# Kernel optimization log

Hardware: AMD Instinct MI355X
Metric: run time of the kernel (lower is better)

The kernel has to match this reference:

```python
import jax, jax.numpy as jnp
import numpy as np
from jax import lax


def _ln(x, gamma, beta, eps=1e-5):
    m = jnp.mean(x, -1, keepdims=True)
    v = jnp.mean(jnp.square(x - m), -1, keepdims=True)
    return (x - m) * lax.rsqrt(v + eps) * gamma + beta


def setup_inputs() -> dict:
    key = jax.random.key(0)
    ks = jax.random.split(key, 12)
    B, C, L = 16, 22, 3000
    D, D2, E, T, K = 64, 256, 8, 4, 13
    s = 0.02
    f32 = jnp.float32
    return dict(
        x_stream=jax.random.normal(ks[0], (B, C, L), f32),
        task_ids=jax.random.randint(ks[1], (B,), 0, T),
        conv_w=jax.random.normal(ks[2], (D, C, K), f32) * s,
        conv_b=jnp.zeros((D,), f32),
        cls_token=jax.random.normal(ks[3], (1, 1, D), f32) * s,
        tok_g=jnp.ones((D,), f32), tok_b=jnp.zeros((D,), f32),
        ds_conv_w=jax.random.normal(ks[4], (D2, 1, 1, K), f32) * s,
        ds_conv_b=jnp.zeros((D2,), f32),
        ds_comp_w=jax.random.normal(ks[5], (D2, D2, D), f32) * s,
        ds_comp_b=jnp.zeros((D2,), f32),
        ds_g=jnp.ones((D2,), f32), ds_b=jnp.zeros((D2,), f32),
        task_embed=jax.random.normal(ks[6], (T, D2), f32) * s,
        gate_w=jax.random.normal(ks[7], (2 * D2, E), f32) * s,
        gate_b=jnp.zeros((E,), f32),
        exp_w=jax.random.normal(ks[8], (E, D2, D2), f32) * s,
        exp_b=jnp.zeros((E, D2), f32),
        uni_w=jax.random.normal(ks[9], (D2, D2), f32) * s,
        uni_b=jnp.zeros((D2,), f32),
        out_g=jnp.ones((D2,), f32), out_b=jnp.zeros((D2,), f32),
    )


def reference(x_stream, task_ids, conv_w, conv_b, cls_token, tok_g, tok_b,
              ds_conv_w, ds_conv_b, ds_comp_w, ds_comp_b, ds_g, ds_b,
              task_embed, gate_w, gate_b, exp_w, exp_b, uni_w, uni_b,
              out_g, out_b):
    gelu = lambda x: jax.nn.gelu(x, approximate=False)
    # --- Tokenize1D: conv1d(stride 2, pad 6) -> GELU -> maxpool(3,3) -> cls cat -> LN
    h = lax.conv_general_dilated(x_stream, conv_w, (2,), [(6, 6)],
                                 dimension_numbers=('NCH', 'OIH', 'NCH')) + conv_b[:, None]
    h = gelu(h)
    h = lax.reduce_window(h, -jnp.inf, lax.max, (1, 1, 3), (1, 1, 3), 'VALID')
    h = jnp.transpose(h, (0, 2, 1))                       # [B, N0, D]
    B = h.shape[0]
    cls = jnp.broadcast_to(cls_token, (B, 1, cls_token.shape[-1]))
    h = jnp.concatenate([cls, h], axis=1)                 # [B, N, D]
    h = _ln(h, tok_g, tok_b)
    # --- DSConvBlock (depth 1): conv2d 1->D2 over (1,13), compress over dim, LN, GELU
    z = jnp.transpose(h, (0, 2, 1))[:, None]              # [B, 1, D, N]
    z = lax.conv_general_dilated(z, ds_conv_w, (1, 1), [(0, 0), (6, 6)],
                                 dimension_numbers=('NCHW', 'OIHW', 'NCHW'))
    z = z + ds_conv_b[:, None, None]                      # [B, D2, D, N]
    z = jnp.einsum('bcdn,ocd->bno', z, ds_comp_w) + ds_comp_b  # compress -> [B, N, D2]
    tokens = gelu(_ln(z, ds_g, ds_b))
    # --- TaskAwareMoE (eval: no dropout, no noise)
    Bn, N, D2 = tokens.shape
    t_vec = task_embed[task_ids]                          # [B, D2]
    T_cat = jnp.concatenate([tokens, jnp.broadcast_to(t_vec[:, None], (Bn, N, D2))], -1)
    logits = T_cat @ gate_w + gate_b                      # [B, N, E]
    topk_vals, topk_idx = lax.top_k(logits, 2)
    gates_k = jax.nn.softmax(topk_vals, axis=-1)          # softmax over top-k (rest are -inf -> 0)
    bi = jnp.arange(Bn)[:, None, None]
    ni = jnp.arange(N)[None, :, None]
    gates = jnp.zeros_like(logits).at[bi, ni, topk_idx].set(gates_k)
    expert_outs = gelu(jnp.einsum('bnd,edf->bnef', tokens, exp_w) + exp_b)  # [B,N,E,D2]
    T_task = jnp.einsum('bne,bnef->bnf', gates, expert_outs)
    T_univ = gelu(tokens @ uni_w + uni_b)
    omega = 1.0 - jnp.max(gates, axis=-1, keepdims=True)
    out = _ln(T_task + omega * T_univ, out_g, out_b)
    return out[:, 0, :]
```

## Files before the change

### kernel.cpp

```cpp
#include <hip/hip_runtime.h>
#include <hip/hip_bf16.h>
#include <math.h>

__device__ __forceinline__ float us2f(unsigned short u) {
    union { unsigned int i; float f; } cv;
    cv.i = ((unsigned int)u) << 16;
    return cv.f;
}

__device__ __forceinline__ int detect_bf(const void* ones_vec) {
    return ((const unsigned int*)ones_vec)[0] == 0x3F803F80u;
}

template<int BF>
__device__ __forceinline__ float ldg(const void* p, int i) {
    return BF ? us2f(((const unsigned short*)p)[i]) : ((const float*)p)[i];
}

__device__ __forceinline__ float wave_sum64(float v) {
#pragma unroll
    for (int m = 32; m > 0; m >>= 1) v += __shfl_xor(v, m, 64);
    return v;
}

__device__ __forceinline__ float gelu_exact(float x) {
    return 0.5f * x * (1.0f + erff(x * 0.7071067811865475f));
}

__device__ __forceinline__ float2 bsum16x2(float a, float b, float* sh32) {
    int lane = threadIdx.x & 63, w = threadIdx.x >> 6;
    a = wave_sum64(a);
    b = wave_sum64(b);
    __syncthreads();
    if (lane == 0) { sh32[w] = a; sh32[16 + w] = b; }
    __syncthreads();
    float s1 = 0, s2 = 0;
#pragma unroll
    for (int i = 0; i < 16; ++i) { s1 += sh32[i]; s2 += sh32[16 + i]; }
    return make_float2(s1, s2);
}

template<int BF>
__device__ void m2_body(float* smembase,
    const void* __restrict__ comp_w, const void* __restrict__ dconv_w,
    const void* __restrict__ dconv_b, const void* __restrict__ comp_b,
    float* __restrict__ M2T, float* __restrict__ BE)
{
    int t = threadIdx.x, w = t >> 6, lane = t & 63;
    float* s_dsw = smembase;
    float* s_dcb = s_dsw + 1792;
    float* sred  = s_dcb + 256;
    for (int i = t; i < 1792; i += 512) {
        int c = i / 7, j = i - c * 7;
        s_dsw[i] = ldg<BF>(dconv_w, c * 13 + 6 + j);
    }
    for (int i = t; i < 256; i += 512) s_dcb[i] = ldg<BF>(dconv_b, i);
    __syncthreads();

    int o = blockIdx.x;
    float a0 = 0, a1 = 0, a2 = 0, a3 = 0, a4 = 0, a5 = 0, a6 = 0, ab = 0;
    int base = o * 16384 + lane;
    int c0 = w * 32;
#pragma unroll 8
    for (int ci = 0; ci < 32; ++ci) {
        int c = c0 + ci;
        float wv = ldg<BF>(comp_w, base + c * 64);
        const float* ds = &s_dsw[c * 7];
        a0 += wv * ds[0]; a1 += wv * ds[1]; a2 += wv * ds[2]; a3 += wv * ds[3];
        a4 += wv * ds[4]; a5 += wv * ds[5]; a6 += wv * ds[6];
        ab += wv * s_dcb[c];
    }
    sred[(w * 8 + 0) * 64 + lane] = a0;
    sred[(w * 8 + 1) * 64 + lane] = a1;
    sred[(w * 8 + 2) * 64 + lane] = a2;
    sred[(w * 8 + 3) * 64 + lane] = a3;
    sred[(w * 8 + 4) * 64 + lane] = a4;
    sred[(w * 8 + 5) * 64 + lane] = a5;
    sred[(w * 8 + 6) * 64 + lane] = a6;
    sred[(w * 8 + 7) * 64 + lane] = ab;
    __syncthreads();
    if (t < 448) {
        int j = t >> 6, d = t & 63;
        float s = 0;
#pragma unroll
        for (int ww = 0; ww < 8; ++ww) s += sred[(ww * 8 + j) * 64 + d];
        M2T[o * 448 + t] = s;
    } else {
        float s = 0;
#pragma unroll
        for (int ww = 0; ww < 8; ++ww) s += sred[(ww * 8 + 7) * 64 + lane];
        s = wave_sum64(s);
        if (lane == 0) BE[o] = ldg<BF>(comp_b, o) + s;
    }
}

__global__ __launch_bounds__(512, 2) void k_m2(
    const void* __restrict__ tok_g,
    const void* __restrict__ comp_w, const void* __restrict__ dconv_w,
    const void* __restrict__ dconv_b, const void* __restrict__ comp_b,
    float* __restrict__ M2T, float* __restrict__ BE)
{
    __shared__ float smem[1792 + 256 + 4096];
    int bf = detect_bf(tok_g);
    if (bf) m2_body<1>(smem, comp_w, dconv_w, dconv_b, comp_b, M2T, BE);
    else    m2_body<0>(smem, comp_w, dconv_w, dconv_b, comp_b, M2T, BE);
}

template<int BF>
__device__ void main_body(char* smem,
    const void* __restrict__ x, const void* __restrict__ conv_w,
    const void* __restrict__ conv_b, const void* __restrict__ cls,
    const void* __restrict__ tok_g, const void* __restrict__ tok_b,
    const float* __restrict__ M2T, const float* __restrict__ BE,
    const int* __restrict__ task_ids,
    const void* __restrict__ ds_g, const void* __restrict__ ds_b,
    const void* __restrict__ task_embed,
    const void* __restrict__ gate_w, const void* __restrict__ gate_b,
    const void* __restrict__ exp_w, const void* __restrict__ exp_b,
    const void* __restrict__ uni_w, const void* __restrict__ uni_b,
    const void* __restrict__ out_g, const void* __restrict__ out_b,
    void* __restrict__ out)
{
    float* sxp    = (float*)smem;
    unsigned int* sw2 = (unsigned int*)(sxp + 1408);
    float* sh_h   = (float*)(sw2 + 10010);
    float* shp0   = sh_h + 448;
    float* shp1   = shp0 + 1024;
    float* shp2   = shp1 + 1024;
    float* sh_tok = shp2 + 1024;
    float* sh32   = sh_tok + 256;
    float* sh_g32 = sh32 + 32;
    float* sh_sc  = sh_g32 + 32;
    int*   sh_e   = (int*)(sh_sc + 4);

    int t = threadIdx.x, b = blockIdx.x;
    int o = t & 255, q = t >> 8, lane = t & 63, w = t >> 6;

    for (int i = t; i < 22 * 64; i += 1024) {
        int c = i >> 6, j = i & 63;
        float v = 0.0f;
        if (j >= 6 && j < 47) v = ldg<BF>(x, (b * 22 + c) * 3000 + (j - 6));
        sxp[i] = v;
    }
    if (BF) {
        const unsigned short* cwu = (const unsigned short*)conv_w;
        for (int i = t; i < 154 * 64; i += 1024) {
            int d = i / 154, ck2 = i - d * 154;
            int c = ck2 / 7, kp = ck2 - c * 7;
            unsigned int lo = cwu[d * 286 + c * 13 + 2 * kp];
            unsigned int hi = (kp < 6) ? cwu[d * 286 + c * 13 + 2 * kp + 1] : 0u;
            sw2[ck2 * 65 + d] = lo | (hi << 16);
        }
    }
    __syncthreads();

    int tt = w - 1;
    float val = 0.0f;
    if (w >= 1 && w <= 6) {
        float cb = ldg<BF>(conv_b, lane);
        float p0 = cb, p1 = cb, p2 = cb;
        if (BF) {
            for (int c = 0; c < 22; ++c) {
                float xv[18];
                const float* xr = &sxp[c * 64 + 6 * tt];
#pragma unroll
                for (int i = 0; i < 8; ++i) {
                    float2 fq = *(const float2*)&xr[2 * i];
                    xv[2 * i] = fq.x; xv[2 * i + 1] = fq.y;
                }
                xv[16] = xr[16];
                xv[17] = 0.0f;
                const unsigned int* wr = &sw2[c * 7 * 65 + lane];
#pragma unroll
                for (int kp = 0; kp < 7; ++kp) {
                    unsigned int pr = wr[kp * 65];
                    float w0 = us2f((unsigned short)(pr & 0xffff));
                    float w1 = us2f((unsigned short)(pr >> 16));
                    p0 += xv[2 * kp]     * w0 + xv[2 * kp + 1] * w1;
                    p1 += xv[2 * kp + 2] * w0 + xv[2 * kp + 3] * w1;
                    p2 += xv[2 * kp + 4] * w0 + xv[2 * kp + 5] * w1;
                }
            }
        } else {
            const float* cwf = (const float*)conv_w;
            for (int c = 0; c < 22; ++c) {
                const float* xr = &sxp[c * 64 + 6 * tt];
                const float* wr = &cwf[lane * 286 + c * 13];
#pragma unroll
                for (int k = 0; k < 13; ++k) {
                    float wv = wr[k];
                    p0 += xr[k] * wv; p1 += xr[k + 2] * wv; p2 += xr[k + 4] * wv;
                }
            }
        }
        val = fmaxf(fmaxf(gelu_exact(p0), gelu_exact(p1)), gelu_exact(p2));
    } else if (w == 0) {
        val = ldg<BF>(cls, lane);
    }
    if (w <= 6) {
        float mean = wave_sum64(val) * (1.0f / 64.0f);
        float dv = val - mean;
        float var = wave_sum64(dv * dv) * (1.0f / 64.0f);
        sh_h[w * 64 + lane] =
            dv * rsqrtf(var + 1e-5f) * ldg<BF>(tok_g, lane) + ldg<BF>(tok_b, lane);
    }
    __syncthreads();

    float p = 0;
    {
        const float4* mrow = (const float4*)&M2T[o * 448 + q * 112];
        const float4* hrow = (const float4*)&sh_h[q * 112];
#pragma unroll 7
        for (int i = 0; i < 28; ++i) {
            float4 m4 = mrow[i];
            float4 h4 = hrow[i];
            p += m4.x * h4.x + m4.y * h4.y + m4.z * h4.z + m4.w * h4.w;
        }
    }
    shp0[q * 256 + o] = p;
    __syncthreads();

    float z = 0;
    if (t < 256)
        z = BE[o] + ((shp0[o] + shp0[256 + o]) + (shp0[512 + o] + shp0[768 + o]));
    float2 ss = bsum16x2(z, z * z, sh32);
    float mean = ss.x * (1.0f / 256.0f);
    float var = ss.y * (1.0f / 256.0f) - mean * mean;
    float rstd = rsqrtf(var + 1e-5f);
    if (t < 256) {
        float tok = gelu_exact((z - mean) * rstd * ldg<BF>(ds_g, o) + ldg<BF>(ds_b, o));
        sh_tok[o] = tok;
    }
    __syncthreads();

    int task = task_ids[b];
    {
        float tko = sh_tok[o];
        float tvo = ldg<BF>(task_embed, task * 256 + o);
        int ea = q * 2, eb = q * 2 + 1;
        float g0p = tko * ldg<BF>(gate_w, o * 8 + ea) + tvo * ldg<BF>(gate_w, (256 + o) * 8 + ea);
        float g1p = tko * ldg<BF>(gate_w, o * 8 + eb) + tvo * ldg<BF>(gate_w, (256 + o) * 8 + eb);
        g0p = wave_sum64(g0p);
        g1p = wave_sum64(g1p);
        if (lane == 0) { sh_g32[w * 2] = g0p; sh_g32[w * 2 + 1] = g1p; }
    }
    __syncthreads();
    if (t == 0) {
        float lg[8];
#pragma unroll
        for (int e = 0; e < 8; ++e) {
            int qq = e >> 1, r = e & 1;
            float s = ldg<BF>(gate_b, e);
#pragma unroll
            for (int i = 0; i < 4; ++i) s += sh_g32[(qq * 4 + i) * 2 + r];
            lg[e] = s;
        }
        int e0 = 0;
        for (int e = 1; e < 8; ++e) if (lg[e] > lg[e0]) e0 = e;
        int e1 = (e0 == 0) ? 1 : 0;
        for (int e = 0; e < 8; ++e) if (e != e0 && lg[e] > lg[e1]) e1 = e;
        float g0 = 1.0f / (1.0f + expf(lg[e1] - lg[e0]));
        sh_sc[0] = g0; sh_sc[1] = 1.0f - g0; sh_sc[2] = 1.0f - g0;
        sh_e[0] = e0; sh_e[1] = e1;
    }
    __syncthreads();
    int e0 = sh_e[0], e1 = sh_e[1];
    float g0 = sh_sc[0], g1 = sh_sc[1], om = sh_sc[2];

    float a0 = 0, a1 = 0, au = 0;
    int d0 = q * 64;
    int b0 = e0 * 65536 + o, b1 = e1 * 65536 + o;
#pragma unroll 16
    for (int i = 0; i < 64; ++i) {
        int d = d0 + i;
        float tk = sh_tok[d];
        a0 += tk * ldg<BF>(exp_w, b0 + d * 256);
        a1 += tk * ldg<BF>(exp_w, b1 + d * 256);
        au += tk * ldg<BF>(uni_w, o + d * 256);
    }
    shp0[q * 256 + o] = a0;
    shp1[q * 256 + o] = a1;
    shp2[q * 256 + o] = au;
    __syncthreads();

    float y = 0;
    if (t < 256) {
        float s0 = ldg<BF>(exp_b, e0 * 256 + o) + ((shp0[o] + shp0[256 + o]) + (shp0[512 + o] + shp0[768 + o]));
        float s1 = ldg<BF>(exp_b, e1 * 256 + o) + ((shp1[o] + shp1[256 + o]) + (shp1[512 + o] + shp1[768 + o]));
        float su = ldg<BF>(uni_b, o)            + ((shp2[o] + shp2[256 + o]) + (shp2[512 + o] + shp2[768 + o]));
        y = g0 * gelu_exact(s0) + g1 * gelu_exact(s1) + om * gelu_exact(su);
    }
    float2 s2v = bsum16x2(y, y * y, sh32);
    float m2v = s2v.x * (1.0f / 256.0f);
    float v2 = s2v.y * (1.0f / 256.0f) - m2v * m2v;
    float rstd2 = rsqrtf(v2 + 1e-5f);
    if (t < 256) {
        float res = (y - m2v) * rstd2 * ldg<BF>(out_g, o) + ldg<BF>(out_b, o);
        if (BF) ((__hip_bfloat16*)out)[b * 256 + o] = __float2bfloat16(res);
        else    ((float*)out)[b * 256 + o] = res;
    }
}

__global__ __launch_bounds__(1024) void k_main(
    const void* __restrict__ x, const void* __restrict__ conv_w,
    const void* __restrict__ conv_b, const void* __restrict__ cls,
    const void* __restrict__ tok_g, const void* __restrict__ tok_b,
    const float* __restrict__ M2T, const float* __restrict__ BE,
    const int* __restrict__ task_ids,
    const void* __restrict__ ds_g, const void* __restrict__ ds_b,
    const void* __restrict__ task_embed,
    const void* __restrict__ gate_w, const void* __restrict__ gate_b,
    const void* __restrict__ exp_w, const void* __restrict__ exp_b,
    const void* __restrict__ uni_w, const void* __restrict__ uni_b,
    const void* __restrict__ out_g, const void* __restrict__ out_b,
    void* __restrict__ out)
{
    __shared__ __align__(16) char smem[(1408 + 10010 + 448 + 3 * 1024 + 256 + 32 + 32 + 4 + 2) * 4 + 16];
    int bf = detect_bf(tok_g);
    if (bf) main_body<1>(smem, x, conv_w, conv_b, cls, tok_g, tok_b, M2T, BE,
                         task_ids, ds_g, ds_b, task_embed, gate_w, gate_b,
                         exp_w, exp_b, uni_w, uni_b, out_g, out_b, out);
    else    main_body<0>(smem, x, conv_w, conv_b, cls, tok_g, tok_b, M2T, BE,
                         task_ids, ds_g, ds_b, task_embed, gate_w, gate_b,
                         exp_w, exp_b, uni_w, uni_b, out_g, out_b, out);
}

extern "C" void kernel_launch(void* const* d_in, const int* in_sizes, int n_in,
                              void* d_out, int out_size, void* d_ws, size_t ws_size,
                              hipStream_t stream) {
    const void* x         = d_in[0];
    const int* task_ids   = (const int*)d_in[1];
    const void* conv_w    = d_in[2];
    const void* conv_b    = d_in[3];
    const void* cls       = d_in[4];
    const void* tok_g     = d_in[5];
    const void* tok_b     = d_in[6];
    const void* ds_conv_w = d_in[7];
    const void* ds_conv_b = d_in[8];
    const void* ds_comp_w = d_in[9];
    const void* ds_comp_b = d_in[10];
    const void* ds_g      = d_in[11];
    const void* ds_b      = d_in[12];
    const void* task_embed= d_in[13];
    const void* gate_w    = d_in[14];
    const void* gate_b    = d_in[15];
    const void* exp_w     = d_in[16];
    const void* exp_b     = d_in[17];
    const void* uni_w     = d_in[18];
    const void* uni_b     = d_in[19];
    const void* out_g     = d_in[20];
    const void* out_b     = d_in[21];

    float* ws = (float*)d_ws;
    float* M2T = ws;
    float* BE  = ws + 114688;

    hipLaunchKernelGGL(k_m2, dim3(256), dim3(512), 0, stream,
                       tok_g, ds_comp_w, ds_conv_w, ds_conv_b, ds_comp_b, M2T, BE);
    hipLaunchKernelGGL(k_main, dim3(16), dim3(1024), 0, stream,
                       x, conv_w, conv_b, cls, tok_g, tok_b, M2T, BE,
                       task_ids, ds_g, ds_b, task_embed, gate_w, gate_b,
                       exp_w, exp_b, uni_w, uni_b, out_g, out_b, d_out);
}
```

Before: 151.1 us.

## Split pipeline into tokenizer, fused compress-projection, and MoE kernels

Restructures the two-kernel pipeline into three. The tokenizer runs first and writes the 7 normalized tokens per batch to workspace. The compress-weight folding kernel then applies each folded row directly to all 16 batches' tokens, producing Z instead of writing the 448x256 folded matrix to global memory. That matrix used to be re-read by every block of the main kernel. The change removes the M2T round trip and the 1024-thread dot-product phase, at the cost of one extra kernel launch and staging H in shared memory per block.

```diff
diff --git a/kernel.cpp b/kernel.cpp
--- a/kernel.cpp
+++ b/kernel.cpp
@@ -41,102 +41,17 @@
 }
 
 template<int BF>
-__device__ void m2_body(float* smembase,
-    const void* __restrict__ comp_w, const void* __restrict__ dconv_w,
-    const void* __restrict__ dconv_b, const void* __restrict__ comp_b,
-    float* __restrict__ M2T, float* __restrict__ BE)
-{
-    int t = threadIdx.x, w = t >> 6, lane = t & 63;
-    float* s_dsw = smembase;
-    float* s_dcb = s_dsw + 1792;
-    float* sred  = s_dcb + 256;
-    for (int i = t; i < 1792; i += 512) {
-        int c = i / 7, j = i - c * 7;
-        s_dsw[i] = ldg<BF>(dconv_w, c * 13 + 6 + j);
-    }
-    for (int i = t; i < 256; i += 512) s_dcb[i] = ldg<BF>(dconv_b, i);
-    __syncthreads();
-
-    int o = blockIdx.x;
-    float a0 = 0, a1 = 0, a2 = 0, a3 = 0, a4 = 0, a5 = 0, a6 = 0, ab = 0;
-    int base = o * 16384 + lane;
-    int c0 = w * 32;
-#pragma unroll 8
-    for (int ci = 0; ci < 32; ++ci) {
-        int c = c0 + ci;
-        float wv = ldg<BF>(comp_w, base + c * 64);
-        const float* ds = &s_dsw[c * 7];
-        a0 += wv * ds[0]; a1 += wv * ds[1]; a2 += wv * ds[2]; a3 += wv * ds[3];
-        a4 += wv * ds[4]; a5 += wv * ds[5]; a6 += wv * ds[6];
-        ab += wv * s_dcb[c];
-    }
-    sred[(w * 8 + 0) * 64 + lane] = a0;
-    sred[(w * 8 + 1) * 64 + lane] = a1;
-    sred[(w * 8 + 2) * 64 + lane] = a2;
-    sred[(w * 8 + 3) * 64 + lane] = a3;
-    sred[(w * 8 + 4) * 64 + lane] = a4;
-    sred[(w * 8 + 5) * 64 + lane] = a5;
-    sred[(w * 8 + 6) * 64 + lane] = a6;
-    sred[(w * 8 + 7) * 64 + lane] = ab;
-    __syncthreads();
-    if (t < 448) {
-        int j = t >> 6, d = t & 63;
-        float s = 0;
-#pragma unroll
-        for (int ww = 0; ww < 8; ++ww) s += sred[(ww * 8 + j) * 64 + d];
-        M2T[o * 448 + t] = s;
-    } else {
-        float s = 0;
-#pragma unroll
-        for (int ww = 0; ww < 8; ++ww) s += sred[(ww * 8 + 7) * 64 + lane];
-        s = wave_sum64(s);
-        if (lane == 0) BE[o] = ldg<BF>(comp_b, o) + s;
-    }
-}
-
-__global__ __launch_bounds__(512, 2) void k_m2(
-    const void* __restrict__ tok_g,
-    const void* __restrict__ comp_w, const void* __restrict__ dconv_w,
-    const void* __restrict__ dconv_b, const void* __restrict__ comp_b,
-    float* __restrict__ M2T, float* __restrict__ BE)
-{
-    __shared__ float smem[1792 + 256 + 4096];
-    int bf = detect_bf(tok_g);
-    if (bf) m2_body<1>(smem, comp_w, dconv_w, dconv_b, comp_b, M2T, BE);
-    else    m2_body<0>(smem, comp_w, dconv_w, dconv_b, comp_b, M2T, BE);
-}
-
-template<int BF>
-__device__ void main_body(char* smem,
+__device__ void tok_body(char* smem,
     const void* __restrict__ x, const void* __restrict__ conv_w,
     const void* __restrict__ conv_b, const void* __restrict__ cls,
     const void* __restrict__ tok_g, const void* __restrict__ tok_b,
-    const float* __restrict__ M2T, const float* __restrict__ BE,
-    const int* __restrict__ task_ids,
-    const void* __restrict__ ds_g, const void* __restrict__ ds_b,
-    const void* __restrict__ task_embed,
-    const void* __restrict__ gate_w, const void* __restrict__ gate_b,
-    const void* __restrict__ exp_w, const void* __restrict__ exp_b,
-    const void* __restrict__ uni_w, const void* __restrict__ uni_b,
-    const void* __restrict__ out_g, const void* __restrict__ out_b,
-    void* __restrict__ out)
-{
-    float* sxp    = (float*)smem;
+    float* __restrict__ H)
+{
+    float* sxp = (float*)smem;
     unsigned int* sw2 = (unsigned int*)(sxp + 1408);
-    float* sh_h   = (float*)(sw2 + 10010);
-    float* shp0   = sh_h + 448;
-    float* shp1   = shp0 + 1024;
-    float* shp2   = shp1 + 1024;
-    float* sh_tok = shp2 + 1024;
-    float* sh32   = sh_tok + 256;
-    float* sh_g32 = sh32 + 32;
-    float* sh_sc  = sh_g32 + 32;
-    int*   sh_e   = (int*)(sh_sc + 4);
-
     int t = threadIdx.x, b = blockIdx.x;
-    int o = t & 255, q = t >> 8, lane = t & 63, w = t >> 6;
-
-    for (int i = t; i < 22 * 64; i += 1024) {
+
+    for (int i = t; i < 22 * 64; i += 448) {
         int c = i >> 6, j = i & 63;
         float v = 0.0f;
         if (j >= 6 && j < 47) v = ldg<BF>(x, (b * 22 + c) * 3000 + (j - 6));
@@ -144,7 +59,7 @@
     }
     if (BF) {
         const unsigned short* cwu = (const unsigned short*)conv_w;
-        for (int i = t; i < 154 * 64; i += 1024) {
+        for (int i = t; i < 154 * 64; i += 448) {
             int d = i / 154, ck2 = i - d * 154;
             int c = ck2 / 7, kp = ck2 - c * 7;
             unsigned int lo = cwu[d * 286 + c * 13 + 2 * kp];
@@ -154,9 +69,9 @@
     }
     __syncthreads();
 
-    int tt = w - 1;
+    int w = t >> 6, lane = t & 63, tt = w - 1;
     float val = 0.0f;
-    if (w >= 1 && w <= 6) {
+    if (w >= 1) {
         float cb = ldg<BF>(conv_b, lane);
         float p0 = cb, p1 = cb, p2 = cb;
         if (BF) {
@@ -194,43 +109,141 @@
             }
         }
         val = fmaxf(fmaxf(gelu_exact(p0), gelu_exact(p1)), gelu_exact(p2));
-    } else if (w == 0) {
+    } else {
         val = ldg<BF>(cls, lane);
     }
-    if (w <= 6) {
-        float mean = wave_sum64(val) * (1.0f / 64.0f);
-        float dv = val - mean;
-        float var = wave_sum64(dv * dv) * (1.0f / 64.0f);
-        sh_h[w * 64 + lane] =
-            dv * rsqrtf(var + 1e-5f) * ldg<BF>(tok_g, lane) + ldg<BF>(tok_b, lane);
-    }
-    __syncthreads();
-
-    float p = 0;
-    {
-        const float4* mrow = (const float4*)&M2T[o * 448 + q * 112];
-        const float4* hrow = (const float4*)&sh_h[q * 112];
-#pragma unroll 7
-        for (int i = 0; i < 28; ++i) {
-            float4 m4 = mrow[i];
-            float4 h4 = hrow[i];
-            p += m4.x * h4.x + m4.y * h4.y + m4.z * h4.z + m4.w * h4.w;
-        }
-    }
-    shp0[q * 256 + o] = p;
-    __syncthreads();
-
-    float z = 0;
-    if (t < 256)
-        z = BE[o] + ((shp0[o] + shp0[256 + o]) + (shp0[512 + o] + shp0[768 + o]));
+    float mean = wave_sum64(val) * (1.0f / 64.0f);
+    float dv = val - mean;
+    float var = wave_sum64(dv * dv) * (1.0f / 64.0f);
+    H[b * 448 + w * 64 + lane] =
+        dv * rsqrtf(var + 1e-5f) * ldg<BF>(tok_g, lane) + ldg<BF>(tok_b, lane);
+}
+
+__global__ __launch_bounds__(448) void k_tok(
+    const void* __restrict__ x, const void* __restrict__ conv_w,
+    const void* __restrict__ conv_b, const void* __restrict__ cls,
+    const void* __restrict__ tok_g, const void* __restrict__ tok_b,
+    float* __restrict__ H)
+{
+    __shared__ __align__(16) char smem[(1408 + 10010) * 4 + 16];
+    int bf = detect_bf(tok_g);
+    if (bf) tok_body<1>(smem, x, conv_w, conv_b, cls, tok_g, tok_b, H);
+    else    tok_body<0>(smem, x, conv_w, conv_b, cls, tok_g, tok_b, H);
+}
+
+template<int BF>
+__device__ void m2z_body(float* smembase,
+    const void* __restrict__ comp_w, const void* __restrict__ dconv_w,
+    const void* __restrict__ dconv_b, const void* __restrict__ comp_b,
+    const float* __restrict__ H, float* __restrict__ Z)
+{
+    int t = threadIdx.x, w = t >> 6, lane = t & 63;
+    float* s_dsw = smembase;
+    float* s_dcb = s_dsw + 1792;
+    float* sred  = s_dcb + 256;
+    float* sH    = sred + 4096;
+    float* row   = sH + 7168;
+    float* sbe   = row + 448;
+
+    for (int i = t; i < 1792; i += 512) {
+        int c = i / 7, j = i - c * 7;
+        s_dsw[i] = ldg<BF>(dconv_w, c * 13 + 6 + j);
+    }
+    for (int i = t; i < 256; i += 512) s_dcb[i] = ldg<BF>(dconv_b, i);
+    for (int i = t; i < 7168; i += 512) sH[i] = H[i];
+    __syncthreads();
+
+    int o = blockIdx.x;
+    float a0 = 0, a1 = 0, a2 = 0, a3 = 0, a4 = 0, a5 = 0, a6 = 0, ab = 0;
+    int base = o * 16384 + lane;
+    int c0 = w * 32;
+#pragma unroll 8
+    for (int ci = 0; ci < 32; ++ci) {
+        int c = c0 + ci;
+        float wv = ldg<BF>(comp_w, base + c * 64);
+        const float* ds = &s_dsw[c * 7];
+        a0 += wv * ds[0]; a1 += wv * ds[1]; a2 += wv * ds[2]; a3 += wv * ds[3];
+        a4 += wv * ds[4]; a5 += wv * ds[5]; a6 += wv * ds[6];
+        ab += wv * s_dcb[c];
+    }
+    sred[(w * 8 + 0) * 64 + lane] = a0;
+    sred[(w * 8 + 1) * 64 + lane] = a1;
+    sred[(w * 8 + 2) * 64 + lane] = a2;
+    sred[(w * 8 + 3) * 64 + lane] = a3;
+    sred[(w * 8 + 4) * 64 + lane] = a4;
+    sred[(w * 8 + 5) * 64 + lane] = a5;
+    sred[(w * 8 + 6) * 64 + lane] = a6;
+    sred[(w * 8 + 7) * 64 + lane] = ab;
+    __syncthreads();
+    if (t < 448) {
+        float s = 0;
+#pragma unroll
+        for (int ww = 0; ww < 8; ++ww) s += sred[(ww * 8 + (t >> 6)) * 64 + (t & 63)];
+        row[t] = s;
+    } else {
+        float s = 0;
+#pragma unroll
+        for (int ww = 0; ww < 8; ++ww) s += sred[(ww * 8 + 7) * 64 + lane];
+        s = wave_sum64(s);
+        if (lane == 0) sbe[0] = ldg<BF>(comp_b, o) + s;
+    }
+    __syncthreads();
+
+    float be = sbe[0];
+#pragma unroll
+    for (int r = 0; r < 2; ++r) {
+        int b = w * 2 + r;
+        const float* hb = &sH[b * 448];
+        float p = 0;
+#pragma unroll
+        for (int i = 0; i < 7; ++i) p += row[lane + 64 * i] * hb[lane + 64 * i];
+        p = wave_sum64(p);
+        if (lane == 0) Z[b * 256 + o] = be + p;
+    }
+}
+
+__global__ __launch_bounds__(512, 2) void k_m2z(
+    const void* __restrict__ tok_g,
+    const void* __restrict__ comp_w, const void* __restrict__ dconv_w,
+    const void* __restrict__ dconv_b, const void* __restrict__ comp_b,
+    const float* __restrict__ H, float* __restrict__ Z)
+{
+    __shared__ float smem[1792 + 256 + 4096 + 7168 + 448 + 8];
+    int bf = detect_bf(tok_g);
+    if (bf) m2z_body<1>(smem, comp_w, dconv_w, dconv_b, comp_b, H, Z);
+    else    m2z_body<0>(smem, comp_w, dconv_w, dconv_b, comp_b, H, Z);
+}
+
+template<int BF>
+__device__ void moe_body(float* smem,
+    const float* __restrict__ Z, const int* __restrict__ task_ids,
+    const void* __restrict__ ds_g, const void* __restrict__ ds_b,
+    const void* __restrict__ task_embed,
+    const void* __restrict__ gate_w, const void* __restrict__ gate_b,
+    const void* __restrict__ exp_w, const void* __restrict__ exp_b,
+    const void* __restrict__ uni_w, const void* __restrict__ uni_b,
+    const void* __restrict__ out_g, const void* __restrict__ out_b,
+    void* __restrict__ out)
+{
+    float* shp0   = smem;
+    float* shp1   = shp0 + 1024;
+    float* shp2   = shp1 + 1024;
+    float* sh_tok = shp2 + 1024;
+    float* sh32   = sh_tok + 256;
+    float* sh_g32 = sh32 + 32;
+    float* sh_sc  = sh_g32 + 32;
+    int*   sh_e   = (int*)(sh_sc + 4);
+
+    int t = threadIdx.x, b = blockIdx.x;
+    int o = t & 255, q = t >> 8, lane = t & 63, w = t >> 6;
+
+    float z = (t < 256) ? Z[b * 256 + o] : 0.0f;
     float2 ss = bsum16x2(z, z * z, sh32);
     float mean = ss.x * (1.0f / 256.0f);
     float var = ss.y * (1.0f / 256.0f) - mean * mean;
     float rstd = rsqrtf(var + 1e-5f);
-    if (t < 256) {
-        float tok = gelu_exact((z - mean) * rstd * ldg<BF>(ds_g, o) + ldg<BF>(ds_b, o));
-        sh_tok[o] = tok;
-    }
+    if (t < 256)
+        sh_tok[o] = gelu_exact((z - mean) * rstd * ldg<BF>(ds_g, o) + ldg<BF>(ds_b, o));
     __syncthreads();
 
     int task = task_ids[b];
@@ -301,12 +314,9 @@
     }
 }
 
-__global__ __launch_bounds__(1024) void k_main(
-    const void* __restrict__ x, const void* __restrict__ conv_w,
-    const void* __restrict__ conv_b, const void* __restrict__ cls,
-    const void* __restrict__ tok_g, const void* __restrict__ tok_b,
-    const float* __restrict__ M2T, const float* __restrict__ BE,
-    const int* __restrict__ task_ids,
+__global__ __launch_bounds__(1024) void k_moe(
+    const float* __restrict__ Z, const int* __restrict__ task_ids,
+    const void* __restrict__ tok_g,
     const void* __restrict__ ds_g, const void* __restrict__ ds_b,
     const void* __restrict__ task_embed,
     const void* __restrict__ gate_w, const void* __restrict__ gate_b,
@@ -315,14 +325,12 @@
     const void* __restrict__ out_g, const void* __restrict__ out_b,
     void* __restrict__ out)
 {
-    __shared__ __align__(16) char smem[(1408 + 10010 + 448 + 3 * 1024 + 256 + 32 + 32 + 4 + 2) * 4 + 16];
+    __shared__ float smem[3 * 1024 + 256 + 32 + 32 + 4 + 4];
     int bf = detect_bf(tok_g);
-    if (bf) main_body<1>(smem, x, conv_w, conv_b, cls, tok_g, tok_b, M2T, BE,
-                         task_ids, ds_g, ds_b, task_embed, gate_w, gate_b,
-                         exp_w, exp_b, uni_w, uni_b, out_g, out_b, out);
-    else    main_body<0>(smem, x, conv_w, conv_b, cls, tok_g, tok_b, M2T, BE,
-                         task_ids, ds_g, ds_b, task_embed, gate_w, gate_b,
-                         exp_w, exp_b, uni_w, uni_b, out_g, out_b, out);
+    if (bf) moe_body<1>(smem, Z, task_ids, ds_g, ds_b, task_embed, gate_w,
+                        gate_b, exp_w, exp_b, uni_w, uni_b, out_g, out_b, out);
+    else    moe_body<0>(smem, Z, task_ids, ds_g, ds_b, task_embed, gate_w,
+                        gate_b, exp_w, exp_b, uni_w, uni_b, out_g, out_b, out);
 }
 
 extern "C" void kernel_launch(void* const* d_in, const int* in_sizes, int n_in,
@@ -352,13 +360,15 @@
     const void* out_b     = d_in[21];
 
     float* ws = (float*)d_ws;
-    float* M2T = ws;
-    float* BE  = ws + 114688;
-
-    hipLaunchKernelGGL(k_m2, dim3(256), dim3(512), 0, stream,
-                       tok_g, ds_comp_w, ds_conv_w, ds_conv_b, ds_comp_b, M2T, BE);
-    hipLaunchKernelGGL(k_main, dim3(16), dim3(1024), 0, stream,
-                       x, conv_w, conv_b, cls, tok_g, tok_b, M2T, BE,
-                       task_ids, ds_g, ds_b, task_embed, gate_w, gate_b,
-                       exp_w, exp_b, uni_w, uni_b, out_g, out_b, d_out);
-}
+    float* H = ws;
+    float* Z = ws + 7168;
+
+    hipLaunchKernelGGL(k_tok, dim3(16), dim3(448), 0, stream,
+                       x, conv_w, conv_b, cls, tok_g, tok_b, H);
+    hipLaunchKernelGGL(k_m2z, dim3(256), dim3(512), 0, stream,
+                       tok_g, ds_comp_w, ds_conv_w, ds_conv_b, ds_comp_b, H, Z);
+    hipLaunchKernelGGL(k_moe, dim3(16), dim3(1024), 0, stream,
+                       Z, task_ids, tok_g, ds_g, ds_b, task_embed,
+                       gate_w, gate_b, exp_w, exp_b, uni_w, uni_b,
+                       out_g, out_b, d_out);
+}
```

New measurement: 145.1 us. 4.0% less time.
